# Performance work log

Hardware: AMD Instinct MI355X
Metric: run time of the kernel (lower is better)

The kernel has to match this reference:

```python
import jax, jax.numpy as jnp
import numpy as np

NEG_INF = -9e15
ALPHA = 0.2  # LeakyReLU negative slope

N = 4096
NFEAT = 512
NHID = 256
NEMBED = 128
NHEADS = 4
OUT1 = NHID // NHEADS   # 64
OUT2 = NEMBED // NHEADS # 32


def _gat_layer(x, adj_mask, W, a):
    # x: [N, F_in]; adj_mask: [N, N] bool; W: [H, F_in, F_out]; a: [H, 2*F_out]
    Fo = W.shape[-1]
    Wh = jnp.einsum('nf,hfo->hno', x, W)                     # [H, N, Fo]
    a_src = jnp.einsum('hno,ho->hn', Wh, a[:, :Fo])          # [H, N]
    a_dst = jnp.einsum('hno,ho->hn', Wh, a[:, Fo:])          # [H, N]
    e = a_src[:, :, None] + a_dst[:, None, :]                # [H, N, N]
    e = jax.nn.leaky_relu(e, negative_slope=ALPHA)
    e = jnp.where(adj_mask[None, :, :], e, NEG_INF)
    att = jax.nn.softmax(e, axis=-1)                         # [H, N, N]
    h = jnp.einsum('hnm,hmo->hno', att, Wh)                  # [H, N, Fo]
    h = jax.nn.elu(h)                                        # concat=True -> ELU
    # concat heads: [N, H*Fo]
    return jnp.transpose(h, (1, 0, 2)).reshape(x.shape[0], -1)


def setup_inputs() -> dict:
    key = jax.random.key(0)
    k1, k2, k3, k4, k5, k6 = jax.random.split(key, 6)
    x = jax.random.normal(k1, (N, NFEAT), dtype=jnp.float32)
    adj = (jax.random.uniform(k2, (N, N)) < 0.01).astype(jnp.float32)
    # per-head GAT params, xavier-uniform-like init (stacked over heads)
    def xavier(k, shape, fan):
        bound = np.sqrt(6.0 / fan)
        return jax.random.uniform(k, shape, minval=-bound, maxval=bound, dtype=jnp.float32)
    W1 = xavier(k3, (NHEADS, NFEAT, OUT1), NFEAT + OUT1)
    a1 = xavier(k4, (NHEADS, 2 * OUT1), 2 * OUT1 + 1)
    W2 = xavier(k5, (NHEADS, NHID, OUT2), NHID + OUT2)
    a2 = xavier(k6, (NHEADS, 2 * OUT2), 2 * OUT2 + 1)
    return {'x': x, 'adj': adj, 'W1': W1, 'a1': a1, 'W2': W2, 'a2': a2}


def reference(x, adj, W1, a1, W2, a2):
    # eval mode: dropout is identity
    adj_mask = adj > 0
    h1 = _gat_layer(x, adj_mask, W1, a1)    # [N, NHID]
    h2 = _gat_layer(h1, adj_mask, W2, a2)   # [N, NEMBED]
    return h2
```

## Files before the change

### kernel.cpp

```cpp
#include <hip/hip_runtime.h>
#include <hip/hip_bf16.h>
#include <cstdint>
#include <cstddef>

#define NNODES 4096
#define NHEADS 4
#define NBR_STRIDE 128

typedef __attribute__((ext_vector_type(8))) short bf16x8v;
typedef __attribute__((ext_vector_type(4))) float f32x4;

__device__ inline unsigned short bf16_rn(float f) {
    unsigned int u = __float_as_uint(f);
    u += 0x7FFFu + ((u >> 16) & 1u);
    return (unsigned short)(u >> 16);
}
__device__ inline float bf16_f32(unsigned short s) {
    return __uint_as_float(((unsigned int)s) << 16);
}

__device__ inline void build_nbr_body(
    const float* __restrict__ adj, int* __restrict__ nbr, int* __restrict__ deg,
    int rowblk) {
    int wave = threadIdx.x >> 6;
    int lane = threadIdx.x & 63;
    int row = rowblk * 4 + wave;
    const float4* arow = reinterpret_cast<const float4*>(adj + (size_t)row * NNODES);
    float4 v[16];
    #pragma unroll
    for (int it = 0; it < 16; ++it) v[it] = arow[it * 64 + lane];
    unsigned long long lt = (1ull << lane) - 1ull;
    int base = 0;
    #pragma unroll
    for (int it = 0; it < 16; ++it) {
        bool b0 = v[it].x > 0.f, b1 = v[it].y > 0.f, b2 = v[it].z > 0.f, b3 = v[it].w > 0.f;
        unsigned long long m0 = __ballot(b0);
        unsigned long long m1 = __ballot(b1);
        unsigned long long m2 = __ballot(b2);
        unsigned long long m3 = __ballot(b3);
        int pre = __popcll(m0 & lt) + __popcll(m1 & lt) +
                  __popcll(m2 & lt) + __popcll(m3 & lt);
        int pos = base + pre;
        int colb = it * 256 + lane * 4;
        if (b0) { if (pos < NBR_STRIDE) nbr[row * NBR_STRIDE + pos] = colb;     pos++; }
        if (b1) { if (pos < NBR_STRIDE) nbr[row * NBR_STRIDE + pos] = colb + 1; pos++; }
        if (b2) { if (pos < NBR_STRIDE) nbr[row * NBR_STRIDE + pos] = colb + 2; pos++; }
        if (b3) { if (pos < NBR_STRIDE) nbr[row * NBR_STRIDE + pos] = colb + 3; pos++; }
        base += __popcll(m0) + __popcll(m1) + __popcll(m2) + __popcll(m3);
    }
    if (lane == 0) deg[row] = base < NBR_STRIDE ? base : NBR_STRIDE;
}

__global__ __launch_bounds__(256) void pack_b_both_kernel(
    const float* __restrict__ W1, const float* __restrict__ W2,
    unsigned short* __restrict__ B1h, unsigned short* __restrict__ B1l,
    unsigned short* __restrict__ B2h, unsigned short* __restrict__ B2l) {
    int t = blockIdx.x * 256 + threadIdx.x;
    if (t < 256 * 512) {
        int n = t >> 9, k = t & 511;
        int h = n >> 6, o = n & 63;
        float v = W1[((size_t)h * 512 + k) * 64 + o];
        unsigned short hi = bf16_rn(v);
        B1h[t] = hi;
        B1l[t] = bf16_rn(v - bf16_f32(hi));
    } else {
        int u = t - 256 * 512;
        if (u < 128 * 256) {
            int n = u >> 8, k = u & 255;
            int h = n >> 5, o = n & 31;
            float v = W2[((size_t)h * 256 + k) * 32 + o];
            unsigned short hi = bf16_rn(v);
            B2h[u] = hi;
            B2l[u] = bf16_rn(v - bf16_f32(hi));
        }
    }
}

template <int K, int N, int FO, int BK, bool ASPLIT>
__device__ inline void gemm_body(
    char* arena,
    const float* __restrict__ A,
    const unsigned short* __restrict__ Ah, const unsigned short* __restrict__ Al,
    const unsigned short* __restrict__ Bh, const unsigned short* __restrict__ Bl,
    const float* __restrict__ a, float* __restrict__ C,
    float* __restrict__ asrc, float* __restrict__ adst,
    int bx, int by) {
    constexpr int BM = 32, BN = 64, LP = BK + 8;
    constexpr int ALD = BM * LP * 2;
    constexpr int BLD = BN * LP * 2;
    typedef unsigned short (*lds_t)[LP];
    lds_t Alh = (lds_t)(arena);
    lds_t All = (lds_t)(arena + ALD);
    lds_t Blh = (lds_t)(arena + 2 * ALD);
    lds_t Bll = (lds_t)(arena + 2 * ALD + BLD);
    float* reds = (float*)(arena + 2 * ALD + 2 * BLD);
    float* redd = (float*)(arena + 2 * ALD + 2 * BLD + 256);
    int tid = threadIdx.x;
    int wave = tid >> 6, lane = tid & 63;
    int rowBase = bx * BM;
    int colBase = by * BN;
    int wr = wave >> 1, wc = wave & 1;
    int lr = lane & 15, lk = lane >> 4;
    f32x4 acc0 = {0.f, 0.f, 0.f, 0.f};
    f32x4 acc1 = {0.f, 0.f, 0.f, 0.f};

    for (int k0 = 0; k0 < K; k0 += BK) {
        if constexpr (BK == 32) {
            int ar = tid >> 3, acf = (tid & 7) * 4;
            int br = tid >> 2, bc = (tid & 3) * 8;
            uint4 bh = *reinterpret_cast<const uint4*>(&Bh[(size_t)(colBase + br) * K + k0 + bc]);
            uint4 bl = *reinterpret_cast<const uint4*>(&Bl[(size_t)(colBase + br) * K + k0 + bc]);
            if constexpr (ASPLIT) {
                uint2 avh = *reinterpret_cast<const uint2*>(&Ah[(size_t)(rowBase + ar) * K + k0 + acf]);
                uint2 avl = *reinterpret_cast<const uint2*>(&Al[(size_t)(rowBase + ar) * K + k0 + acf]);
                __syncthreads();
                *reinterpret_cast<uint2*>(&Alh[ar][acf]) = avh;
                *reinterpret_cast<uint2*>(&All[ar][acf]) = avl;
                *reinterpret_cast<uint4*>(&Blh[br][bc]) = bh;
                *reinterpret_cast<uint4*>(&Bll[br][bc]) = bl;
            } else {
                float4 a0 = *reinterpret_cast<const float4*>(&A[(size_t)(rowBase + ar) * K + k0 + acf]);
                __syncthreads();
                ushort4 h4, l4;
                h4.x = bf16_rn(a0.x); l4.x = bf16_rn(a0.x - bf16_f32(h4.x));
                h4.y = bf16_rn(a0.y); l4.y = bf16_rn(a0.y - bf16_f32(h4.y));
                h4.z = bf16_rn(a0.z); l4.z = bf16_rn(a0.z - bf16_f32(h4.z));
                h4.w = bf16_rn(a0.w); l4.w = bf16_rn(a0.w - bf16_f32(h4.w));
                *reinterpret_cast<ushort4*>(&Alh[ar][acf]) = h4;
                *reinterpret_cast<ushort4*>(&All[ar][acf]) = l4;
                *reinterpret_cast<uint4*>(&Blh[br][bc]) = bh;
                *reinterpret_cast<uint4*>(&Bll[br][bc]) = bl;
            }
        } else {
            int ar = tid >> 3, ac = (tid & 7) * 8;
            uint4 bh0 = *reinterpret_cast<const uint4*>(&Bh[(size_t)(colBase + ar) * K + k0 + ac]);
            uint4 bl0 = *reinterpret_cast<const uint4*>(&Bl[(size_t)(colBase + ar) * K + k0 + ac]);
            uint4 bh1 = *reinterpret_cast<const uint4*>(&Bh[(size_t)(colBase + 32 + ar) * K + k0 + ac]);
            uint4 bl1 = *reinterpret_cast<const uint4*>(&Bl[(size_t)(colBase + 32 + ar) * K + k0 + ac]);
            if constexpr (ASPLIT) {
                uint4 avh = *reinterpret_cast<const uint4*>(&Ah[(size_t)(rowBase + ar) * K + k0 + ac]);
                uint4 avl = *reinterpret_cast<const uint4*>(&Al[(size_t)(rowBase + ar) * K + k0 + ac]);
                __syncthreads();
                *reinterpret_cast<uint4*>(&Alh[ar][ac]) = avh;
                *reinterpret_cast<uint4*>(&All[ar][ac]) = avl;
                *reinterpret_cast<uint4*>(&Blh[ar][ac]) = bh0;
                *reinterpret_cast<uint4*>(&Bll[ar][ac]) = bl0;
                *reinterpret_cast<uint4*>(&Blh[32 + ar][ac]) = bh1;
                *reinterpret_cast<uint4*>(&Bll[32 + ar][ac]) = bl1;
            } else {
                float4 a0 = *reinterpret_cast<const float4*>(&A[(size_t)(rowBase + ar) * K + k0 + ac]);
                float4 a1 = *reinterpret_cast<const float4*>(&A[(size_t)(rowBase + ar) * K + k0 + ac + 4]);
                __syncthreads();
                ushort4 h4, l4;
                h4.x = bf16_rn(a0.x); l4.x = bf16_rn(a0.x - bf16_f32(h4.x));
                h4.y = bf16_rn(a0.y); l4.y = bf16_rn(a0.y - bf16_f32(h4.y));
                h4.z = bf16_rn(a0.z); l4.z = bf16_rn(a0.z - bf16_f32(h4.z));
                h4.w = bf16_rn(a0.w); l4.w = bf16_rn(a0.w - bf16_f32(h4.w));
                *reinterpret_cast<ushort4*>(&Alh[ar][ac]) = h4;
                *reinterpret_cast<ushort4*>(&All[ar][ac]) = l4;
                h4.x = bf16_rn(a1.x); l4.x = bf16_rn(a1.x - bf16_f32(h4.x));
                h4.y = bf16_rn(a1.y); l4.y = bf16_rn(a1.y - bf16_f32(h4.y));
                h4.z = bf16_rn(a1.z); l4.z = bf16_rn(a1.z - bf16_f32(h4.z));
                h4.w = bf16_rn(a1.w); l4.w = bf16_rn(a1.w - bf16_f32(h4.w));
                *reinterpret_cast<ushort4*>(&Alh[ar][ac + 4]) = h4;
                *reinterpret_cast<ushort4*>(&All[ar][ac + 4]) = l4;
                *reinterpret_cast<uint4*>(&Blh[ar][ac]) = bh0;
                *reinterpret_cast<uint4*>(&Bll[ar][ac]) = bl0;
                *reinterpret_cast<uint4*>(&Blh[32 + ar][ac]) = bh1;
                *reinterpret_cast<uint4*>(&Bll[32 + ar][ac]) = bl1;
            }
        }
        __syncthreads();
        #pragma unroll
        for (int ks = 0; ks < BK / 32; ++ks) {
            int kb = ks * 32 + lk * 8;
            bf16x8v ah = *reinterpret_cast<const bf16x8v*>(&Alh[wr * 16 + lr][kb]);
            bf16x8v al = *reinterpret_cast<const bf16x8v*>(&All[wr * 16 + lr][kb]);
            bf16x8v b0h = *reinterpret_cast<const bf16x8v*>(&Blh[wc * 32 + lr][kb]);
            bf16x8v b0l = *reinterpret_cast<const bf16x8v*>(&Bll[wc * 32 + lr][kb]);
            bf16x8v b1h = *reinterpret_cast<const bf16x8v*>(&Blh[wc * 32 + 16 + lr][kb]);
            bf16x8v b1l = *reinterpret_cast<const bf16x8v*>(&Bll[wc * 32 + 16 + lr][kb]);
            acc0 = __builtin_amdgcn_mfma_f32_16x16x32_bf16(ah, b0h, acc0, 0, 0, 0);
            acc0 = __builtin_amdgcn_mfma_f32_16x16x32_bf16(ah, b0l, acc0, 0, 0, 0);
            acc0 = __builtin_amdgcn_mfma_f32_16x16x32_bf16(al, b0h, acc0, 0, 0, 0);
            acc1 = __builtin_amdgcn_mfma_f32_16x16x32_bf16(ah, b1h, acc1, 0, 0, 0);
            acc1 = __builtin_amdgcn_mfma_f32_16x16x32_bf16(ah, b1l, acc1, 0, 0, 0);
            acc1 = __builtin_amdgcn_mfma_f32_16x16x32_bf16(al, b1h, acc1, 0, 0, 0);
        }
    }
    int crow = rowBase + wr * 16 + lk * 4;
    int ccol = colBase + wc * 32 + lr;
    #pragma unroll
    for (int r = 0; r < 4; ++r) {
        C[(size_t)(crow + r) * N + ccol]      = acc0[r];
        C[(size_t)(crow + r) * N + ccol + 16] = acc1[r];
    }
    int n0 = colBase + wc * 32 + lr;
    int hh = n0 / FO;
    int o0 = n0 % FO;
    int o1 = o0 + 16;
    const float* av = a + hh * 2 * FO;
    float aS0 = av[o0], aS1 = av[o1];
    float aD0 = av[FO + o0], aD1 = av[FO + o1];
    float sv[4], dv[4];
    #pragma unroll
    for (int r = 0; r < 4; ++r) {
        sv[r] = acc0[r] * aS0 + acc1[r] * aS1;
        dv[r] = acc0[r] * aD0 + acc1[r] * aD1;
        #pragma unroll
        for (int msk = 1; msk < 16; msk <<= 1) {
            sv[r] += __shfl_xor(sv[r], msk);
            dv[r] += __shfl_xor(dv[r], msk);
        }
    }
    if constexpr (FO == 64) {
        if (lr == 0) {
            #pragma unroll
            for (int r = 0; r < 4; ++r) {
                reds[wc * 32 + wr * 16 + lk * 4 + r] = sv[r];
                redd[wc * 32 + wr * 16 + lk * 4 + r] = dv[r];
            }
        }
        __syncthreads();
        if (tid < BM) {
            int row = tid;
            asrc[(size_t)(rowBase + row) * NHEADS + by] = reds[row] + reds[32 + row];
            adst[(size_t)(rowBase + row) * NHEADS + by] = redd[row] + redd[32 + row];
        }
    } else {
        if (lr == 0) {
            #pragma unroll
            for (int r = 0; r < 4; ++r) {
                int row = rowBase + wr * 16 + lk * 4 + r;
                asrc[(size_t)row * NHEADS + hh] = sv[r];
                adst[(size_t)row * NHEADS + hh] = dv[r];
            }
        }
    }
}

__global__ __launch_bounds__(256) void fused1_kernel(
    const float* __restrict__ adj, int* __restrict__ nbr, int* __restrict__ deg,
    const float* __restrict__ x,
    const unsigned short* __restrict__ B1h, const unsigned short* __restrict__ B1l,
    const float* __restrict__ a1, float* __restrict__ Wh1,
    float* __restrict__ as1, float* __restrict__ ad1) {
    __shared__ __align__(16) char arena[15872];
    int b = blockIdx.x;
    if (b < 512) {
        gemm_body<512, 256, 64, 32, false>(arena, x, nullptr, nullptr,
                                           B1h, B1l, a1, Wh1, as1, ad1,
                                           b & 127, b >> 7);
    } else {
        build_nbr_body(adj, nbr, deg, b - 512);
    }
}

__global__ __launch_bounds__(256) void gemm2_kernel(
    const unsigned short* __restrict__ Ah, const unsigned short* __restrict__ Al,
    const unsigned short* __restrict__ Bh, const unsigned short* __restrict__ Bl,
    const float* __restrict__ a, float* __restrict__ C,
    float* __restrict__ asrc, float* __restrict__ adst) {
    __shared__ __align__(16) char arena[28160];
    gemm_body<256, 128, 32, 64, true>(arena, nullptr, Ah, Al, Bh, Bl,
                                      a, C, asrc, adst, blockIdx.x, blockIdx.y);
}

template <int FO, bool SPLITOUT>
__global__ __launch_bounds__(256) void agg_kernel(
    const float* __restrict__ Wh,
    const float* __restrict__ asrc, const float* __restrict__ adst,
    const int* __restrict__ nbr, const int* __restrict__ deg,
    float* __restrict__ out,
    unsigned short* __restrict__ outh, unsigned short* __restrict__ outl) {
    __shared__ float2 sw[4][NBR_STRIDE];
    int wslot = threadIdx.x >> 6;
    int lane = threadIdx.x & 63;
    int n = blockIdx.x;
    int h = wslot;
    int dg = deg[n];
    const int* lst = nbr + n * NBR_STRIDE;
    float my_as = asrc[(size_t)n * NHEADS + h];

    int c0 = 0, c1 = 0;
    float e0 = -1e30f, e1 = -1e30f;
    if (lane < dg) {
        c0 = lst[lane];
        float e = my_as + adst[(size_t)c0 * NHEADS + h];
        e0 = e >= 0.f ? e : 0.2f * e;
    }
    if (lane + 64 < dg) {
        c1 = lst[lane + 64];
        float e = my_as + adst[(size_t)c1 * NHEADS + h];
        e1 = e >= 0.f ? e : 0.2f * e;
    }
    float m = fmaxf(e0, e1);
    #pragma unroll
    for (int s = 32; s; s >>= 1) m = fmaxf(m, __shfl_xor(m, s));
    float p0 = (lane < dg) ? __expf(e0 - m) : 0.f;
    float p1 = (lane + 64 < dg) ? __expf(e1 - m) : 0.f;
    float denom = p0 + p1;
    #pragma unroll
    for (int s = 32; s; s >>= 1) denom += __shfl_xor(denom, s);
    float inv = 1.0f / denom;

    if (lane < dg)      sw[wslot][lane]      = make_float2(p0 * inv, __int_as_float(c0));
    if (lane + 64 < dg) sw[wslot][lane + 64] = make_float2(p1 * inv, __int_as_float(c1));

    constexpr int STRIDE = NHEADS * FO;
    constexpr int LPR = FO / 4;
    constexpr int NPS = 64 / LPR;
    int sub = lane / LPR;
    int dim4 = (lane % LPR) * 4;
    const float* whp = Wh + h * FO + dim4;
    f32x4 acc = {0.f, 0.f, 0.f, 0.f};
    int main_n = (dg / (8 * NPS)) * (8 * NPS);
    int k = 0;
    for (; k < main_n; k += 8 * NPS) {
        #pragma unroll
        for (int u = 0; u < 8; ++u) {
            float2 w = sw[wslot][k + u * NPS + sub];
            int col = __float_as_int(w.y);
            float4 v = *reinterpret_cast<const float4*>(&whp[(size_t)col * STRIDE]);
            acc[0] += w.x * v.x;
            acc[1] += w.x * v.y;
            acc[2] += w.x * v.z;
            acc[3] += w.x * v.w;
        }
    }
    #pragma unroll
    for (int u = 0; u < 8; ++u) {
        int kk = main_n + u * NPS + sub;
        if (kk < dg) {
            float2 w = sw[wslot][kk];
            int col = __float_as_int(w.y);
            float4 v = *reinterpret_cast<const float4*>(&whp[(size_t)col * STRIDE]);
            acc[0] += w.x * v.x;
            acc[1] += w.x * v.y;
            acc[2] += w.x * v.z;
            acc[3] += w.x * v.w;
        }
    }
    #pragma unroll
    for (int s = LPR; s < 64; s <<= 1) {
        acc[0] += __shfl_xor(acc[0], s);
        acc[1] += __shfl_xor(acc[1], s);
        acc[2] += __shfl_xor(acc[2], s);
        acc[3] += __shfl_xor(acc[3], s);
    }
    if (lane < LPR) {
        float r0 = acc[0] > 0.f ? acc[0] : expm1f(acc[0]);
        float r1 = acc[1] > 0.f ? acc[1] : expm1f(acc[1]);
        float r2 = acc[2] > 0.f ? acc[2] : expm1f(acc[2]);
        float r3 = acc[3] > 0.f ? acc[3] : expm1f(acc[3]);
        size_t idx = (size_t)n * STRIDE + h * FO + dim4;
        if constexpr (SPLITOUT) {
            ushort4 hv, lv;
            hv.x = bf16_rn(r0); lv.x = bf16_rn(r0 - bf16_f32(hv.x));
            hv.y = bf16_rn(r1); lv.y = bf16_rn(r1 - bf16_f32(hv.y));
            hv.z = bf16_rn(r2); lv.z = bf16_rn(r2 - bf16_f32(hv.z));
            hv.w = bf16_rn(r3); lv.w = bf16_rn(r3 - bf16_f32(hv.w));
            *reinterpret_cast<ushort4*>(&outh[idx]) = hv;
            *reinterpret_cast<ushort4*>(&outl[idx]) = lv;
        } else {
            *reinterpret_cast<float4*>(&out[idx]) = make_float4(r0, r1, r2, r3);
        }
    }
}

extern "C" void kernel_launch(void* const* d_in, const int* in_sizes, int n_in,
                              void* d_out, int out_size, void* d_ws, size_t ws_size,
                              hipStream_t stream) {
    const float* x   = (const float*)d_in[0];
    const float* adj = (const float*)d_in[1];
    const float* W1  = (const float*)d_in[2];
    const float* a1  = (const float*)d_in[3];
    const float* W2  = (const float*)d_in[4];
    const float* a2  = (const float*)d_in[5];
    float* outp = (float*)d_out;

    char* p = (char*)d_ws;
    auto alloc = [&](size_t bytes) -> void* {
        void* r = (void*)p;
        p += (bytes + 255) & ~(size_t)255;
        return r;
    };
    int*   nbr = (int*)alloc((size_t)NNODES * NBR_STRIDE * 4);
    int*   deg = (int*)alloc((size_t)NNODES * 4);
    unsigned short* B1h = (unsigned short*)alloc((size_t)256 * 512 * 2);
    unsigned short* B1l = (unsigned short*)alloc((size_t)256 * 512 * 2);
    unsigned short* B2h = (unsigned short*)alloc((size_t)128 * 256 * 2);
    unsigned short* B2l = (unsigned short*)alloc((size_t)128 * 256 * 2);
    float* Wh1 = (float*)alloc((size_t)NNODES * 256 * 4);
    float* as1 = (float*)alloc((size_t)NHEADS * NNODES * 4);
    float* ad1 = (float*)alloc((size_t)NHEADS * NNODES * 4);
    unsigned short* h1h = (unsigned short*)alloc((size_t)NNODES * 256 * 2);
    unsigned short* h1l = (unsigned short*)alloc((size_t)NNODES * 256 * 2);
    float* Wh2 = (float*)alloc((size_t)NNODES * 128 * 4);
    float* as2 = (float*)alloc((size_t)NHEADS * NNODES * 4);
    float* ad2 = (float*)alloc((size_t)NHEADS * NNODES * 4);

    pack_b_both_kernel<<<dim3((256 * 512 + 128 * 256) / 256), dim3(256), 0, stream>>>(
        W1, W2, B1h, B1l, B2h, B2l);
    fused1_kernel<<<dim3(512 + NNODES / 4), dim3(256), 0, stream>>>(
        adj, nbr, deg, x, B1h, B1l, a1, Wh1, as1, ad1);
    agg_kernel<64, true><<<dim3(NNODES), dim3(256), 0, stream>>>(
        Wh1, as1, ad1, nbr, deg, nullptr, h1h, h1l);
    gemm2_kernel<<<dim3(NNODES / 32, 2), dim3(256), 0, stream>>>(
        h1h, h1l, B2h, B2l, a2, Wh2, as2, ad2);
    agg_kernel<32, false><<<dim3(NNODES), dim3(256), 0, stream>>>(
        Wh2, as2, ad2, nbr, deg, outp, nullptr, nullptr);
}
```

Baseline: 65.67 us.

## Fuse softmax into aggregation with per-lane online softmax and merge

Replaces the two-phase softmax-then-aggregate scheme (compute normalized weights into shared memory, then gather) with a single streaming loop. Each lane group keeps a running max, sum and accumulator, and the partial states are merged across lanes with shuffle reductions. This removes the shared-memory staging and the separate max/sum reductions so the gathers can start immediately. In exchange it adds extra exp and rescale work per neighbor and per merge step.

```diff
diff --git a/kernel.cpp b/kernel.cpp
--- a/kernel.cpp
+++ b/kernel.cpp
@@ -273,7 +273,6 @@
     const int* __restrict__ nbr, const int* __restrict__ deg,
     float* __restrict__ out,
     unsigned short* __restrict__ outh, unsigned short* __restrict__ outl) {
-    __shared__ float2 sw[4][NBR_STRIDE];
     int wslot = threadIdx.x >> 6;
     int lane = threadIdx.x & 63;
     int n = blockIdx.x;
@@ -282,77 +281,80 @@
     const int* lst = nbr + n * NBR_STRIDE;
     float my_as = asrc[(size_t)n * NHEADS + h];
 
-    int c0 = 0, c1 = 0;
-    float e0 = -1e30f, e1 = -1e30f;
-    if (lane < dg) {
-        c0 = lst[lane];
-        float e = my_as + adst[(size_t)c0 * NHEADS + h];
-        e0 = e >= 0.f ? e : 0.2f * e;
-    }
-    if (lane + 64 < dg) {
-        c1 = lst[lane + 64];
-        float e = my_as + adst[(size_t)c1 * NHEADS + h];
-        e1 = e >= 0.f ? e : 0.2f * e;
-    }
-    float m = fmaxf(e0, e1);
-    #pragma unroll
-    for (int s = 32; s; s >>= 1) m = fmaxf(m, __shfl_xor(m, s));
-    float p0 = (lane < dg) ? __expf(e0 - m) : 0.f;
-    float p1 = (lane + 64 < dg) ? __expf(e1 - m) : 0.f;
-    float denom = p0 + p1;
-    #pragma unroll
-    for (int s = 32; s; s >>= 1) denom += __shfl_xor(denom, s);
-    float inv = 1.0f / denom;
-
-    if (lane < dg)      sw[wslot][lane]      = make_float2(p0 * inv, __int_as_float(c0));
-    if (lane + 64 < dg) sw[wslot][lane + 64] = make_float2(p1 * inv, __int_as_float(c1));
-
     constexpr int STRIDE = NHEADS * FO;
     constexpr int LPR = FO / 4;
     constexpr int NPS = 64 / LPR;
     int sub = lane / LPR;
     int dim4 = (lane % LPR) * 4;
     const float* whp = Wh + h * FO + dim4;
+
+    float m = -1e30f, s = 0.f;
     f32x4 acc = {0.f, 0.f, 0.f, 0.f};
-    int main_n = (dg / (8 * NPS)) * (8 * NPS);
-    int k = 0;
-    for (; k < main_n; k += 8 * NPS) {
-        #pragma unroll
-        for (int u = 0; u < 8; ++u) {
-            float2 w = sw[wslot][k + u * NPS + sub];
-            int col = __float_as_int(w.y);
-            float4 v = *reinterpret_cast<const float4*>(&whp[(size_t)col * STRIDE]);
-            acc[0] += w.x * v.x;
-            acc[1] += w.x * v.y;
-            acc[2] += w.x * v.z;
-            acc[3] += w.x * v.w;
-        }
+
+    int k = sub;
+    for (; k + NPS < dg; k += 2 * NPS) {
+        int cA = lst[k];
+        int cB = lst[k + NPS];
+        float eA = my_as + adst[(size_t)cA * NHEADS + h];
+        float eB = my_as + adst[(size_t)cB * NHEADS + h];
+        eA = eA >= 0.f ? eA : 0.2f * eA;
+        eB = eB >= 0.f ? eB : 0.2f * eB;
+        float4 vA = *reinterpret_cast<const float4*>(&whp[(size_t)cA * STRIDE]);
+        float4 vB = *reinterpret_cast<const float4*>(&whp[(size_t)cB * STRIDE]);
+        float mn = fmaxf(m, fmaxf(eA, eB));
+        float sc = __expf(m - mn);
+        float pA = __expf(eA - mn);
+        float pB = __expf(eB - mn);
+        s = s * sc + pA + pB;
+        acc[0] = acc[0] * sc + pA * vA.x + pB * vB.x;
+        acc[1] = acc[1] * sc + pA * vA.y + pB * vB.y;
+        acc[2] = acc[2] * sc + pA * vA.z + pB * vB.z;
+        acc[3] = acc[3] * sc + pA * vA.w + pB * vB.w;
+        m = mn;
+    }
+    if (k < dg) {
+        int c = lst[k];
+        float e = my_as + adst[(size_t)c * NHEADS + h];
+        e = e >= 0.f ? e : 0.2f * e;
+        float4 v = *reinterpret_cast<const float4*>(&whp[(size_t)c * STRIDE]);
+        float mn = fmaxf(m, e);
+        float sc = __expf(m - mn);
+        float p = __expf(e - mn);
+        s = s * sc + p;
+        acc[0] = acc[0] * sc + p * v.x;
+        acc[1] = acc[1] * sc + p * v.y;
+        acc[2] = acc[2] * sc + p * v.z;
+        acc[3] = acc[3] * sc + p * v.w;
+        m = mn;
     }
     #pragma unroll
-    for (int u = 0; u < 8; ++u) {
-        int kk = main_n + u * NPS + sub;
-        if (kk < dg) {
-            float2 w = sw[wslot][kk];
-            int col = __float_as_int(w.y);
-            float4 v = *reinterpret_cast<const float4*>(&whp[(size_t)col * STRIDE]);
-            acc[0] += w.x * v.x;
-            acc[1] += w.x * v.y;
-            acc[2] += w.x * v.z;
-            acc[3] += w.x * v.w;
-        }
-    }
-    #pragma unroll
-    for (int s = LPR; s < 64; s <<= 1) {
-        acc[0] += __shfl_xor(acc[0], s);
-        acc[1] += __shfl_xor(acc[1], s);
-        acc[2] += __shfl_xor(acc[2], s);
-        acc[3] += __shfl_xor(acc[3], s);
+    for (int off = LPR; off < 64; off <<= 1) {
+        float m2 = __shfl_xor(m, off);
+        float s2 = __shfl_xor(s, off);
+        float a0 = __shfl_xor(acc[0], off);
+        float a1 = __shfl_xor(acc[1], off);
+        float a2 = __shfl_xor(acc[2], off);
+        float a3 = __shfl_xor(acc[3], off);
+        float mn = fmaxf(m, m2);
+        float sa = __expf(m - mn);
+        float sb = __expf(m2 - mn);
+        s = s * sa + s2 * sb;
+        acc[0] = acc[0] * sa + a0 * sb;
+        acc[1] = acc[1] * sa + a1 * sb;
+        acc[2] = acc[2] * sa + a2 * sb;
+        acc[3] = acc[3] * sa + a3 * sb;
+        m = mn;
     }
     if (lane < LPR) {
-        float r0 = acc[0] > 0.f ? acc[0] : expm1f(acc[0]);
-        float r1 = acc[1] > 0.f ? acc[1] : expm1f(acc[1]);
-        float r2 = acc[2] > 0.f ? acc[2] : expm1f(acc[2]);
-        float r3 = acc[3] > 0.f ? acc[3] : expm1f(acc[3]);
+        float inv = 1.0f / s;
+        float r0 = acc[0] * inv;
+        float r1 = acc[1] * inv;
+        float r2 = acc[2] * inv;
+        float r3 = acc[3] * inv;
+        r0 = r0 > 0.f ? r0 : expm1f(r0);
+        r1 = r1 > 0.f ? r1 : expm1f(r1);
+        r2 = r2 > 0.f ? r2 : expm1f(r2);
+        r3 = r3 > 0.f ? r3 : expm1f(r3);
         size_t idx = (size_t)n * STRIDE + h * FO + dim4;
         if constexpr (SPLITOUT) {
             ushort4 hv, lv;
```

After: 64.95 us. No clear change (-1.1%).
